# Performance work log

Measured on AMD Instinct MI355X. Metric: run time of the kernel, lower is better.

## Reference

```python
import jax, jax.numpy as jnp
import numpy as np

D_MODEL = 256
N_HEADS = 8
HEAD_DIM = D_MODEL // N_HEADS  # 32
N_LEVELS = 4
N_POINTS = 4
LEVEL_SHAPES = [(100, 100), (50, 50), (25, 25), (13, 13)]
LEVEL_STARTS = [0] + list(np.cumsum([h * w for h, w in LEVEL_SHAPES]))[:-1]
LEN_IN = int(sum(h * w for h, w in LEVEL_SHAPES))  # 13294
BATCH = 2
LEN_Q = LEN_IN  # encoder self-attention


def _offset_bias():
    # faithful to MSDeformAttn._reset_parameters for sampling_offsets bias
    thetas = np.arange(N_HEADS, dtype=np.float32) * (2.0 * np.pi / N_HEADS)
    grid = np.stack([np.cos(thetas), np.sin(thetas)], -1)
    grid = grid / np.abs(grid).max(-1, keepdims=True)
    grid = np.tile(grid.reshape(N_HEADS, 1, 1, 2), (1, N_LEVELS, N_POINTS, 1))
    for i in range(N_POINTS):
        grid[:, :, i, :] *= i + 1
    return jnp.asarray(grid.reshape(-1), dtype=jnp.float32)


def setup_inputs() -> dict:
    key = jax.random.key(0)
    ks = jax.random.split(key, 10)
    s = 1.0 / np.sqrt(D_MODEL)
    inp = {
        "query": jax.random.normal(ks[0], (BATCH, LEN_Q, D_MODEL), jnp.float32),
        "reference_points": jax.random.uniform(ks[1], (BATCH, LEN_Q, N_LEVELS, 2), jnp.float32),
        "input_flatten": jax.random.normal(ks[2], (BATCH, LEN_IN, D_MODEL), jnp.float32),
        "input_spatial_shapes": jnp.asarray(LEVEL_SHAPES, dtype=jnp.int32),
        "W_value": jax.random.normal(ks[3], (D_MODEL, D_MODEL), jnp.float32) * s,
        "b_value": jnp.zeros((D_MODEL,), jnp.float32),
        "W_off": jax.random.normal(ks[4], (D_MODEL, N_HEADS * N_LEVELS * N_POINTS * 2), jnp.float32) * 0.01,
        "b_off": _offset_bias(),
        "W_attn": jax.random.normal(ks[5], (D_MODEL, N_HEADS * N_LEVELS * N_POINTS), jnp.float32) * 0.01,
        "b_attn": jnp.zeros((N_HEADS * N_LEVELS * N_POINTS,), jnp.float32),
        "W_out": jax.random.normal(ks[6], (D_MODEL, D_MODEL), jnp.float32) * s,
        "b_out": jnp.zeros((D_MODEL,), jnp.float32),
    }
    return inp


def _corner(v_t, ix, iy, h, w):
    # v_t: (n, M, h*w, D); ix/iy: (n, M, LqP) int32. Zero padding outside.
    valid = (ix >= 0) & (ix < w) & (iy >= 0) & (iy < h)
    idx = jnp.clip(iy, 0, h - 1) * w + jnp.clip(ix, 0, w - 1)
    g = jnp.take_along_axis(v_t, idx[..., None], axis=2)  # (n, M, LqP, D)
    return g * valid[..., None].astype(v_t.dtype)


def _ms_deform_attn(query, reference_points, input_flatten,
                    W_value, b_value, W_off, b_off, W_attn, b_attn, W_out, b_out):
    n, lq, _ = query.shape
    value = (input_flatten @ W_value + b_value).reshape(n, LEN_IN, N_HEADS, HEAD_DIM)
    offs = (query @ W_off + b_off).reshape(n, lq, N_HEADS, N_LEVELS, N_POINTS, 2)
    aw = jax.nn.softmax(
        (query @ W_attn + b_attn).reshape(n, lq, N_HEADS, N_LEVELS * N_POINTS), axis=-1
    ).reshape(n, lq, N_HEADS, N_LEVELS, N_POINTS)
    # offset_normalizer = (w, h) per level
    norm = jnp.asarray([[w, h] for h, w in LEVEL_SHAPES], dtype=query.dtype)
    loc = reference_points[:, :, None, :, None, :] + offs / norm[None, None, None, :, None, :]

    acc = jnp.zeros((n, N_HEADS, lq, HEAD_DIM), dtype=value.dtype)
    for l, (h, w) in enumerate(LEVEL_SHAPES):
        s0 = LEVEL_STARTS[l]
        v_t = jnp.transpose(value[:, s0:s0 + h * w], (0, 2, 1, 3))  # (n, M, hw, D)
        ll = loc[:, :, :, l]  # (n, lq, M, P, 2) in [0,1]
        # grid_sample bilinear, align_corners=False: pixel = coord*size - 0.5
        x = ll[..., 0] * w - 0.5
        y = ll[..., 1] * h - 0.5
        x0 = jnp.floor(x); y0 = jnp.floor(y)
        tx = x - x0; ty = y - y0
        ix0 = x0.astype(jnp.int32); iy0 = y0.astype(jnp.int32)
        flat = lambda a: jnp.transpose(a, (0, 2, 1, 3)).reshape(n, N_HEADS, lq * N_POINTS)
        ix0f, iy0f = flat(ix0), flat(iy0)
        txf = flat(tx)[..., None]; tyf = flat(ty)[..., None]
        g00 = _corner(v_t, ix0f, iy0f, h, w)
        g01 = _corner(v_t, ix0f + 1, iy0f, h, w)
        g10 = _corner(v_t, ix0f, iy0f + 1, h, w)
        g11 = _corner(v_t, ix0f + 1, iy0f + 1, h, w)
        samp = (g00 * (1 - txf) * (1 - tyf) + g01 * txf * (1 - tyf)
                + g10 * (1 - txf) * tyf + g11 * txf * tyf)
        samp = samp.reshape(n, N_HEADS, lq, N_POINTS, HEAD_DIM)
        wl = jnp.transpose(aw[:, :, :, l], (0, 2, 1, 3))[..., None]  # (n, M, lq, P, 1)
        acc = acc + (samp * wl).sum(axis=3)

    out = jnp.transpose(acc, (0, 2, 1, 3)).reshape(n, lq, D_MODEL)
    return out @ W_out + b_out


def reference(query, reference_points, input_flatten, input_spatial_shapes,
              W_value, b_value, W_off, b_off, W_attn, b_attn, W_out, b_out):
    # input_spatial_shapes carried for signature fidelity; level geometry is static.
    return _ms_deform_attn(query, reference_points, input_flatten,
                           W_value, b_value, W_off, b_off, W_attn, b_attn, W_out, b_out)
```

## Files before the change

kernel.cpp:

```cpp
#include <hip/hip_runtime.h>

#define NH 8
#define HD 32
#define NL 4
#define NP 4
#define DM 256
#define LEN_IN_C 13294
#define LQ_C 13294
#define B_C 2
#define M_TOTAL (B_C * LQ_C)
#define MT_TILES 1662
#define GQ 32
#define QBLKS 831

typedef __attribute__((ext_vector_type(8))) short short8;
typedef __attribute__((ext_vector_type(4))) float floatx4;
typedef __attribute__((ext_vector_type(2))) float floatx2;

__device__ __forceinline__ unsigned short f2bf(float x) {
    union { float f; unsigned int u; } a; a.f = x;
    unsigned int r = (a.u + 0x7FFFu + ((a.u >> 16) & 1u)) >> 16;
    return (unsigned short)r;
}
__device__ __forceinline__ floatx2 up2(unsigned int u) {
    union { unsigned int u; float f; } lo, hi;
    lo.u = u << 16; hi.u = u & 0xffff0000u;
    floatx2 r; r.x = lo.f; r.y = hi.f; return r;
}
__device__ __forceinline__ unsigned int cvtpk_bf16(float lo, float hi) {
    unsigned int r;
    asm("v_cvt_pk_bf16_f32 %0, %1, %2" : "=v"(r) : "v"(lo), "v"(hi));
    return r;
}

__device__ __forceinline__ void conv_b_body(const float* __restrict__ W,
                                            unsigned short* __restrict__ Bsw,
                                            int Nsrc, int NTsrc, int NTtotal, int ntOff,
                                            int vblk) {
    const int u = vblk * 256 + threadIdx.x;
    const int lane = u & 63;
    const int unit = u >> 6;
    const int ntl = unit % NTsrc;
    const int kc = unit / NTsrc;
    const int n = ntl * 16 + (lane & 15);
    const int k0 = kc * 32 + (lane >> 4) * 8;
    short8 v;
#pragma unroll
    for (int j = 0; j < 8; ++j)
        v[j] = (short)f2bf(W[(size_t)(k0 + j) * Nsrc + n]);
    ((short8*)Bsw)[(size_t)(kc * NTtotal + ntOff + ntl) * 64 + lane] = v;
}

__global__ __launch_bounds__(256) void conv_weights_kernel(const float* __restrict__ Wv,
                                                           const float* __restrict__ Woff,
                                                           const float* __restrict__ Wattn,
                                                           const float* __restrict__ Wout,
                                                           const float* __restrict__ boff,
                                                           const float* __restrict__ battn,
                                                           unsigned short* __restrict__ BswV,
                                                           unsigned short* __restrict__ BswOA,
                                                           unsigned short* __restrict__ BswO,
                                                           float* __restrict__ fbias,
                                                           unsigned short* __restrict__ value,
                                                           unsigned short* __restrict__ AccSw) {
    const int blk = blockIdx.x;
    if (blk < 32)        conv_b_body(Wv,    BswV,  256, 16, 16, 0,  blk);
    else if (blk < 64)   conv_b_body(Woff,  BswOA, 256, 16, 24, 0,  blk - 32);
    else if (blk < 80)   conv_b_body(Wattn, BswOA, 128,  8, 24, 16, blk - 64);
    else if (blk < 112)  conv_b_body(Wout,  BswO,  256, 16, 16, 0,  blk - 80);
    else if (blk < 114) {
        const int t = (blk - 112) * 256 + threadIdx.x;
        if (t < 384) fbias[t] = (t < 256) ? boff[t] : battn[t - 256];
        else if (t < 416) {
            const int j = t - 384;
            value[-32 + j] = 0;
            value[(size_t)M_TOTAL * 256 + j] = 0;
        }
    } else {
        const int idx = threadIdx.x;
        if (idx < 128) {
            const int kc = idx >> 4;
            const int sub = idx & 15;
            const int lane = (12 + (sub & 3)) + 16 * (sub >> 2);
            const size_t unit = (size_t)(1661 * 8 + kc) * 64 + lane;
            short8 z = (short8){0, 0, 0, 0, 0, 0, 0, 0};
            ((short8*)AccSw)[unit] = z;
        }
    }
}

template <int NT, int OUTMODE>
__device__ __forceinline__ void gemm_f32a_body(const float* __restrict__ A,
                                               const unsigned short* __restrict__ Bsw,
                                               const float* __restrict__ bias,
                                               void* __restrict__ Cout, int M, int rt) {
    constexpr int NTW = NT / 4;
    const int tid = threadIdx.x;
    const int lane = tid & 63;
    const int wave = tid >> 6;
    const int m = lane & 15;
    const int q = lane >> 4;

    const float* Ar = A + (size_t)min(rt * 16 + m, M - 1) * 256 + q * 8;
    const short8* Bu = (const short8*)Bsw;

    floatx4 acc[NTW];
#pragma unroll
    for (int t = 0; t < NTW; ++t) acc[t] = (floatx4){0.f, 0.f, 0.f, 0.f};

#pragma unroll 2
    for (int kc = 0; kc < 8; ++kc) {
        const float4 f0 = *(const float4*)(Ar + kc * 32);
        const float4 f1 = *(const float4*)(Ar + kc * 32 + 4);
        union { uint4 u; short8 s; } c;
        c.u.x = cvtpk_bf16(f0.x, f0.y); c.u.y = cvtpk_bf16(f0.z, f0.w);
        c.u.z = cvtpk_bf16(f1.x, f1.y); c.u.w = cvtpk_bf16(f1.z, f1.w);
        const short8 a = c.s;
#pragma unroll
        for (int t = 0; t < NTW; ++t) {
            const short8 b = Bu[(size_t)(kc * NT + wave * NTW + t) * 64 + lane];
            acc[t] = __builtin_amdgcn_mfma_f32_16x16x32_bf16(a, b, acc[t], 0, 0, 0);
        }
    }

    const int N = NT * 16;
    const int colq = lane & 15;
    const int rowq = (lane >> 4) * 4;
#pragma unroll
    for (int t = 0; t < NTW; ++t) {
        const int col = (wave * NTW + t) * 16 + colq;
        const float bc = bias[col];
#pragma unroll
        for (int reg = 0; reg < 4; ++reg) {
            const int row = rt * 16 + rowq + reg;
            if (row < M) {
                const float v = acc[t][reg] + bc;
                if (OUTMODE == 1) {
                    const int bb = row >= LEN_IN_C;
                    const int pos = row - (bb ? LEN_IN_C : 0);
                    const int hh = col >> 5;
                    const int dd = col & 31;
                    ((unsigned short*)Cout)[((size_t)((bb << 3) + hh) * LEN_IN_C + pos) * 32 + dd] = f2bf(v);
                } else {
                    ((float*)Cout)[(size_t)row * N + col] = v;
                }
            }
        }
    }
}

__global__ __launch_bounds__(256) void front_gemm_kernel(const float* __restrict__ inflat,
                                                         const float* __restrict__ query,
                                                         const unsigned short* __restrict__ BswV,
                                                         const unsigned short* __restrict__ BswOA,
                                                         const float* __restrict__ bv,
                                                         const float* __restrict__ fbias,
                                                         unsigned short* __restrict__ value,
                                                         float* __restrict__ fused, int M) {
    const int x = blockIdx.x;
    const int rt = x >> 1;
    if ((x & 1) == 0)
        gemm_f32a_body<16, 1>(inflat, BswV, bv, (void*)value, M, rt);
    else
        gemm_f32a_body<24, 0>(query, BswOA, fbias, (void*)fused, M, rt);
}

__global__ __launch_bounds__(256) void back_gemm_kernel(const unsigned short* __restrict__ Asw,
                                                        const unsigned short* __restrict__ Bsw,
                                                        const float* __restrict__ bias,
                                                        float* __restrict__ Cout, int M) {
    constexpr int NT = 16;
    constexpr int NTW = 4;
    const int tid = threadIdx.x;
    const int lane = tid & 63;
    const int wave = tid >> 6;
    const int rt = blockIdx.x;

    const short8* Au = (const short8*)Asw;
    const short8* Bu = (const short8*)Bsw;

    floatx4 acc[NTW];
#pragma unroll
    for (int t = 0; t < NTW; ++t) acc[t] = (floatx4){0.f, 0.f, 0.f, 0.f};

#pragma unroll 2
    for (int kc = 0; kc < 8; ++kc) {
        const short8 a = Au[(size_t)(rt * 8 + kc) * 64 + lane];
#pragma unroll
        for (int t = 0; t < NTW; ++t) {
            const short8 b = Bu[(size_t)(kc * NT + wave * NTW + t) * 64 + lane];
            acc[t] = __builtin_amdgcn_mfma_f32_16x16x32_bf16(a, b, acc[t], 0, 0, 0);
        }
    }

    const int colq = lane & 15;
    const int rowq = (lane >> 4) * 4;
#pragma unroll
    for (int t = 0; t < NTW; ++t) {
        const int col = (wave * NTW + t) * 16 + colq;
        const float bc = bias[col];
#pragma unroll
        for (int reg = 0; reg < 4; ++reg) {
            const int row = rt * 16 + rowq + reg;
            if (row < M)
                Cout[(size_t)row * 256 + col] = acc[t][reg] + bc;
        }
    }
}

__global__ __launch_bounds__(256, 8) void msda_sample_kernel(const float* __restrict__ refp,
                                                             const unsigned short* __restrict__ value,
                                                             const float* __restrict__ fused,
                                                             unsigned short* __restrict__ AccSw) {
    constexpr int lvl_hw[4] = {100, 50, 25, 13};
    constexpr int lvl_s[4] = {0, 10000, 12500, 13125};

    const int wg = blockIdx.x;
    const int h = wg & 7;
    const int q0 = (wg >> 3) * GQ;
    const int tid = threadIdx.x;

    __shared__ float s_ref[GQ * 8];
    __shared__ int2 s_pi[GQ * 17];
    __shared__ float4 s_pw[GQ * 17];

    s_ref[tid] = refp[min(q0 * 8 + tid, M_TOTAL * 8 - 1)];
    __syncthreads();

#pragma unroll
    for (int jj = 0; jj < 2; ++jj) {
        const int job = jj * 256 + tid;
        const int qq = job >> 4;
        const int t16 = job & 15;
        const int l = t16 >> 2;
        const int bq = min(q0 + qq, M_TOTAL - 1);
        const int b = (bq >= LQ_C) ? 1 : 0;

        const float logit = fused[(size_t)bq * 384 + 256 + h * 16 + t16];
        float m = logit;
#pragma unroll
        for (int mask = 1; mask < 16; mask <<= 1) m = fmaxf(m, __shfl_xor(m, mask));
        const float e = expf(logit - m);
        float s = e;
#pragma unroll
        for (int mask = 1; mask < 16; mask <<= 1) s += __shfl_xor(s, mask);
        const float aw = e / s;

        const int whl = lvl_hw[l];
        const float fwh = (float)whl;
        const float2 oxy = *(const float2*)(fused + (size_t)bq * 384 + (h * 16 + t16) * 2);
        const float x = s_ref[qq * 8 + l * 2] * fwh + oxy.x - 0.5f;
        const float y = s_ref[qq * 8 + l * 2 + 1] * fwh + oxy.y - 0.5f;
        const float x0f = floorf(x), y0f = floorf(y);
        const float tx = x - x0f, ty = y - y0f;
        const int ix0 = (int)x0f, iy0 = (int)y0f;

        const bool xv0 = (unsigned)ix0 < (unsigned)whl;
        const bool xv1 = (unsigned)(ix0 + 1) < (unsigned)whl;
        const bool yv0 = (unsigned)iy0 < (unsigned)whl;
        const bool yv1 = (unsigned)(iy0 + 1) < (unsigned)whl;

        const int cxp = min(max(ix0, -1), whl - 1);
        const int cy0 = min(max(iy0, 0), whl - 1);
        const int cy1 = min(max(iy0 + 1, 0), whl - 1);

        const int posb = (b * 8 + h) * LEN_IN_C + lvl_s[l];
        int2 aa;
        aa.x = (posb + cy0 * whl + cxp) * 64;
        aa.y = (posb + cy1 * whl + cxp) * 64;
        float4 wv;
        wv.x = (xv0 && yv0) ? aw * (1.f - tx) * (1.f - ty) : 0.f;
        wv.y = (xv1 && yv0) ? aw * tx * (1.f - ty) : 0.f;
        wv.z = (xv0 && yv1) ? aw * (1.f - tx) * ty : 0.f;
        wv.w = (xv1 && yv1) ? aw * tx * ty : 0.f;
        const int slot = qq * 17 + t16;
        s_pi[slot] = aa;
        s_pw[slot] = wv;
    }
    __syncthreads();

    const int qq = tid >> 3;
    const int l8 = tid & 7;
    const char* vbp = (const char*)value + l8 * 16;
    const int pbase = qq * 17;
    const bool right = (l8 & 4) != 0;

    floatx2 acc0 = (floatx2){0.f, 0.f}, acc1 = acc0, acc2 = acc0, acc3 = acc0;
#pragma unroll 2
    for (int pt = 0; pt < 16; ++pt) {
        const int2 aa = s_pi[pbase + pt];
        const float4 wv = s_pw[pbase + pt];
        const float wt = right ? wv.y : wv.x;
        const float wb = right ? wv.w : wv.z;
        const uint4 vt = *(const uint4*)(vbp + aa.x);
        const uint4 vbm = *(const uint4*)(vbp + aa.y);
        const floatx2 w2t = (floatx2){wt, wt};
        const floatx2 w2b = (floatx2){wb, wb};
        acc0 += w2t * up2(vt.x);
        acc1 += w2t * up2(vt.y);
        acc2 += w2t * up2(vt.z);
        acc3 += w2t * up2(vt.w);
        acc0 += w2b * up2(vbm.x);
        acc1 += w2b * up2(vbm.y);
        acc2 += w2b * up2(vbm.z);
        acc3 += w2b * up2(vbm.w);
    }

    float r0 = acc0.x, r1 = acc0.y, r2 = acc1.x, r3 = acc1.y;
    float r4 = acc2.x, r5 = acc2.y, r6 = acc3.x, r7 = acc3.y;
    r0 += __shfl_xor(r0, 4); r1 += __shfl_xor(r1, 4);
    r2 += __shfl_xor(r2, 4); r3 += __shfl_xor(r3, 4);
    r4 += __shfl_xor(r4, 4); r5 += __shfl_xor(r5, 4);
    r6 += __shfl_xor(r6, 4); r7 += __shfl_xor(r7, 4);

    const int bq = q0 + qq;
    if (!right && bq < M_TOTAL) {
        const int rt = bq >> 4, mm = bq & 15;
        const int unit = (rt * 8 + h) * 64 + ((l8 & 3) * 16 + mm);
        uint4 o;
        o.x = cvtpk_bf16(r0, r1);
        o.y = cvtpk_bf16(r2, r3);
        o.z = cvtpk_bf16(r4, r5);
        o.w = cvtpk_bf16(r6, r7);
        *(uint4*)(AccSw + (size_t)unit * 8) = o;
    }
}

extern "C" void kernel_launch(void* const* d_in, const int* in_sizes, int n_in,
                              void* d_out, int out_size, void* d_ws, size_t ws_size,
                              hipStream_t stream) {
    const float* query  = (const float*)d_in[0];
    const float* refp   = (const float*)d_in[1];
    const float* inflat = (const float*)d_in[2];
    const float* Wv    = (const float*)d_in[4];
    const float* bv    = (const float*)d_in[5];
    const float* Woff  = (const float*)d_in[6];
    const float* boff  = (const float*)d_in[7];
    const float* Wattn = (const float*)d_in[8];
    const float* battn = (const float*)d_in[9];
    const float* Wout  = (const float*)d_in[10];
    const float* bout  = (const float*)d_in[11];
    float* out = (float*)d_out;

    char* p = (char*)d_ws;
    unsigned short* AccSw = (unsigned short*)p;
    p += (size_t)MT_TILES * 8 * 64 * 8 * sizeof(unsigned short);
    unsigned short* BswV = (unsigned short*)p;   p += (size_t)8 * 16 * 64 * 8 * 2;
    unsigned short* BswOA = (unsigned short*)p;  p += (size_t)8 * 24 * 64 * 8 * 2;
    unsigned short* BswO = (unsigned short*)p;   p += (size_t)8 * 16 * 64 * 8 * 2;
    float* fbias = (float*)p;                    p += 384 * sizeof(float);
    unsigned short* value = (unsigned short*)p + 32;
    p += ((size_t)M_TOTAL * 256 + 64) * sizeof(unsigned short);
    float* fused = (float*)p;                    p += (size_t)M_TOTAL * 384 * 4;

    const int M = M_TOTAL;

    conv_weights_kernel<<<115, 256, 0, stream>>>(Wv, Woff, Wattn, Wout, boff, battn,
                                                 BswV, BswOA, BswO, fbias, value, AccSw);
    front_gemm_kernel<<<MT_TILES * 2, 256, 0, stream>>>(inflat, query, BswV, BswOA,
                                                        bv, fbias, value, fused, M);
    msda_sample_kernel<<<QBLKS * 8, 256, 0, stream>>>(refp, value, fused, AccSw);
    back_gemm_kernel<<<MT_TILES, 256, 0, stream>>>(AccSw, BswO, bout, out, M);
}
```

Before: 221.8 us.

## Stage 32-row A tiles in swizzled LDS and reuse each B fragment twice

The front GEMM now cooperatively loads a 32x256 fp32 A tile, converts it to bf16 and stores it into XOR-swizzled shared memory. Each wave then computes two 16-row MFMA tiles per B fragment, halving the number of B-weight loads per output row and halving the block count. Accumulator register use doubles and a barrier plus 16KB of LDS per block are added, which may reduce occupancy.

```diff
diff --git a/kernel.cpp b/kernel.cpp
--- a/kernel.cpp
+++ b/kernel.cpp
@@ -10,6 +10,7 @@
 #define B_C 2
 #define M_TOTAL (B_C * LQ_C)
 #define MT_TILES 1662
+#define RT32_TILES 831
 #define GQ 32
 #define QBLKS 831
 
@@ -90,36 +91,54 @@
 }
 
 template <int NT, int OUTMODE>
-__device__ __forceinline__ void gemm_f32a_body(const float* __restrict__ A,
-                                               const unsigned short* __restrict__ Bsw,
-                                               const float* __restrict__ bias,
-                                               void* __restrict__ Cout, int M, int rt) {
+__device__ __forceinline__ void gemm_lds_full(unsigned short* __restrict__ sA,
+                                              const float* __restrict__ A,
+                                              const unsigned short* __restrict__ Bsw,
+                                              const float* __restrict__ bias,
+                                              void* __restrict__ Cout, int M, int rt32) {
     constexpr int NTW = NT / 4;
     const int tid = threadIdx.x;
     const int lane = tid & 63;
     const int wave = tid >> 6;
+    const int trow = rt32 * 32;
+
+#pragma unroll
+    for (int i = 0; i < 8; ++i) {
+        const int li = i * 1024 + tid * 4;
+        const int lrow = li >> 8;
+        const int lcol = li & 255;
+        const int srow = min(trow + lrow, M - 1);
+        const float4 f = *(const float4*)(A + (size_t)srow * 256 + lcol);
+        uint2 pk;
+        pk.x = cvtpk_bf16(f.x, f.y);
+        pk.y = cvtpk_bf16(f.z, f.w);
+        const int lb = (li * 2) ^ ((lrow & 7) << 4);
+        *(uint2*)((char*)sA + lb) = pk;
+    }
+    __syncthreads();
+
     const int m = lane & 15;
     const int q = lane >> 4;
-
-    const float* Ar = A + (size_t)min(rt * 16 + m, M - 1) * 256 + q * 8;
     const short8* Bu = (const short8*)Bsw;
 
-    floatx4 acc[NTW];
-#pragma unroll
-    for (int t = 0; t < NTW; ++t) acc[t] = (floatx4){0.f, 0.f, 0.f, 0.f};
-
+    floatx4 acc[2][NTW];
+#pragma unroll
+    for (int r = 0; r < 2; ++r)
+#pragma unroll
+        for (int t = 0; t < NTW; ++t) acc[r][t] = (floatx4){0.f, 0.f, 0.f, 0.f};
+
+    const int swz = (m & 7) << 4;
 #pragma unroll 2
     for (int kc = 0; kc < 8; ++kc) {
-        const float4 f0 = *(const float4*)(Ar + kc * 32);
-        const float4 f1 = *(const float4*)(Ar + kc * 32 + 4);
-        union { uint4 u; short8 s; } c;
-        c.u.x = cvtpk_bf16(f0.x, f0.y); c.u.y = cvtpk_bf16(f0.z, f0.w);
-        c.u.z = cvtpk_bf16(f1.x, f1.y); c.u.w = cvtpk_bf16(f1.z, f1.w);
-        const short8 a = c.s;
+        const int fb0 = (m * 512 + kc * 64 + q * 16) ^ swz;
+        const int fb1 = ((m + 16) * 512 + kc * 64 + q * 16) ^ swz;
+        const short8 a0 = *(const short8*)((const char*)sA + fb0);
+        const short8 a1 = *(const short8*)((const char*)sA + fb1);
 #pragma unroll
         for (int t = 0; t < NTW; ++t) {
             const short8 b = Bu[(size_t)(kc * NT + wave * NTW + t) * 64 + lane];
-            acc[t] = __builtin_amdgcn_mfma_f32_16x16x32_bf16(a, b, acc[t], 0, 0, 0);
+            acc[0][t] = __builtin_amdgcn_mfma_f32_16x16x32_bf16(a0, b, acc[0][t], 0, 0, 0);
+            acc[1][t] = __builtin_amdgcn_mfma_f32_16x16x32_bf16(a1, b, acc[1][t], 0, 0, 0);
         }
     }
 
@@ -131,18 +150,21 @@
         const int col = (wave * NTW + t) * 16 + colq;
         const float bc = bias[col];
 #pragma unroll
-        for (int reg = 0; reg < 4; ++reg) {
-            const int row = rt * 16 + rowq + reg;
-            if (row < M) {
-                const float v = acc[t][reg] + bc;
-                if (OUTMODE == 1) {
-                    const int bb = row >= LEN_IN_C;
-                    const int pos = row - (bb ? LEN_IN_C : 0);
-                    const int hh = col >> 5;
-                    const int dd = col & 31;
-                    ((unsigned short*)Cout)[((size_t)((bb << 3) + hh) * LEN_IN_C + pos) * 32 + dd] = f2bf(v);
-                } else {
-                    ((float*)Cout)[(size_t)row * N + col] = v;
+        for (int r = 0; r < 2; ++r) {
+#pragma unroll
+            for (int reg = 0; reg < 4; ++reg) {
+                const int row = trow + r * 16 + rowq + reg;
+                if (row < M) {
+                    const float v = acc[r][t][reg] + bc;
+                    if (OUTMODE == 1) {
+                        const int bb = row >= LEN_IN_C;
+                        const int pos = row - (bb ? LEN_IN_C : 0);
+                        const int hh = col >> 5;
+                        const int dd = col & 31;
+                        ((unsigned short*)Cout)[((size_t)((bb << 3) + hh) * LEN_IN_C + pos) * 32 + dd] = f2bf(v);
+                    } else {
+                        ((float*)Cout)[(size_t)row * N + col] = v;
+                    }
                 }
             }
         }
@@ -157,12 +179,13 @@
                                                          const float* __restrict__ fbias,
                                                          unsigned short* __restrict__ value,
                                                          float* __restrict__ fused, int M) {
+    __shared__ unsigned short sA[32 * 256];
     const int x = blockIdx.x;
-    const int rt = x >> 1;
+    const int rt32 = x >> 1;
     if ((x & 1) == 0)
-        gemm_f32a_body<16, 1>(inflat, BswV, bv, (void*)value, M, rt);
+        gemm_lds_full<16, 1>(sA, inflat, BswV, bv, (void*)value, M, rt32);
     else
-        gemm_f32a_body<24, 0>(query, BswOA, fbias, (void*)fused, M, rt);
+        gemm_lds_full<24, 0>(sA, query, BswOA, fbias, (void*)fused, M, rt32);
 }
 
 __global__ __launch_bounds__(256) void back_gemm_kernel(const unsigned short* __restrict__ Asw,
@@ -357,8 +380,8 @@
 
     conv_weights_kernel<<<115, 256, 0, stream>>>(Wv, Woff, Wattn, Wout, boff, battn,
                                                  BswV, BswOA, BswO, fbias, value, AccSw);
-    front_gemm_kernel<<<MT_TILES * 2, 256, 0, stream>>>(inflat, query, BswV, BswOA,
-                                                        bv, fbias, value, fused, M);
+    front_gemm_kernel<<<RT32_TILES * 2, 256, 0, stream>>>(inflat, query, BswV, BswOA,
+                                                          bv, fbias, value, fused, M);
     msda_sample_kernel<<<QBLKS * 8, 256, 0, stream>>>(refp, value, fused, AccSw);
     back_gemm_kernel<<<MT_TILES, 256, 0, stream>>>(AccSw, BswO, bout, out, M);
 }
```

Result: faster. 195.0 us (-12.1%).
